# Optimization experiments

Measured on AMD Instinct MI355X. Metric: run time of the kernel, lower is better.

## Reference

```python
import jax, jax.numpy as jnp
import numpy as np

MODEL_DIM = 768
NUM_HEADS = 12
HEAD_DIM = MODEL_DIM // NUM_HEADS
TEMPERATURE = 1.0


def setup_inputs() -> dict:
    key = jax.random.key(0)
    ks = jax.random.split(key, 14)
    B, S, M, D = 4, 2048, 512, MODEL_DIM
    scale = 0.02
    return {
        "query_hidden_states": jax.random.normal(ks[0], (B, S, D), jnp.float32),
        "memory_embeddings": jax.random.normal(ks[1], (B, M, D), jnp.float32),
        "memory_scores": jax.random.normal(ks[2], (B, M), jnp.float32),
        "Wq": jax.random.normal(ks[3], (D, D), jnp.float32) * scale,
        "bq": jnp.zeros((D,), jnp.float32),
        "Wk": jax.random.normal(ks[4], (D, D), jnp.float32) * scale,
        "bk": jnp.zeros((D,), jnp.float32),
        "Wv": jax.random.normal(ks[5], (D, D), jnp.float32) * scale,
        "bv": jnp.zeros((D,), jnp.float32),
        "Wo": jax.random.normal(ks[6], (D, D), jnp.float32) * scale,
        "bo": jnp.zeros((D,), jnp.float32),
        "Wg": jax.random.normal(ks[7], (2 * D, D), jnp.float32) * scale,
        "bg": jnp.zeros((D,), jnp.float32),
    }


def reference(query_hidden_states, memory_embeddings, memory_scores,
              Wq, bq, Wk, bk, Wv, bv, Wo, bo, Wg, bg):
    B, S, D = query_hidden_states.shape
    M = memory_embeddings.shape[1]
    H, Hd = NUM_HEADS, HEAD_DIM

    q = query_hidden_states @ Wq + bq            # [B,S,D]
    k = memory_embeddings @ Wk + bk              # [B,M,D]
    v = memory_embeddings @ Wv + bv              # [B,M,D]

    q = q.reshape(B, S, H, Hd).transpose(0, 2, 1, 3) / jnp.sqrt(jnp.float32(Hd))
    k = k.reshape(B, M, H, Hd).transpose(0, 2, 1, 3)
    v = v.reshape(B, M, H, Hd).transpose(0, 2, 1, 3)

    scores = jnp.einsum('bhsd,bhmd->bhsm', q, k) / TEMPERATURE
    # additive memory-score bias broadcast over heads and query positions
    scores = scores + memory_scores[:, None, None, :]
    attn = jax.nn.softmax(scores, axis=-1)       # [B,H,S,M]

    out = jnp.einsum('bhsm,bhmd->bhsd', attn, v)
    out = out.transpose(0, 2, 1, 3).reshape(B, S, D)
    out = out @ Wo + bo                          # [B,S,D]

    concat = jnp.concatenate([query_hidden_states, out], axis=-1)  # [B,S,2D]
    gate = jax.nn.sigmoid(concat @ Wg + bg)
    return gate * out + (1.0 - gate) * query_hidden_states
```

## Files before the change

### kernel.cpp

```cpp
#include <hip/hip_runtime.h>
#include <hip/hip_bf16.h>

#define DEV static __device__ __forceinline__

typedef __attribute__((ext_vector_type(4))) float f32x4;
typedef __attribute__((ext_vector_type(8))) short bf16x8;

DEV unsigned short f2bf(float f) {
  union { float f; unsigned u; } v; v.f = f;
  unsigned r = (v.u + 0x7fffu + ((v.u >> 16) & 1u)) >> 16;
  return (unsigned short)r;
}
DEV float bf2f(unsigned short u) {
  union { unsigned u; float f; } v; v.u = ((unsigned)u) << 16;
  return v.f;
}
DEV void gl_lds16(const unsigned short* g, unsigned short* l) {
  __builtin_amdgcn_global_load_lds(
      (const __attribute__((address_space(1))) void*)g,
      (__attribute__((address_space(3))) void*)l, 16, 0, 0);
}

__global__ void k_cast2(const float* __restrict__ q, unsigned short* __restrict__ concat,
                        const float* __restrict__ mem, unsigned short* __restrict__ mem_bf) {
  int i = blockIdx.x * 256 + threadIdx.x;
  union { unsigned short u[4]; uint2 p; } o;
  if (i < 6144 * 256) {
    const int idx = i * 4;
    const int r = idx / 768, c = idx - r * 768;
    const float4 v = *(const float4*)(q + idx);
    o.u[0] = f2bf(v.x); o.u[1] = f2bf(v.y); o.u[2] = f2bf(v.z); o.u[3] = f2bf(v.w);
    *(uint2*)(concat + (size_t)r * 1536 + c) = o.p;
  } else {
    const int idx = (i - 6144 * 256) * 4;
    const float4 v = *(const float4*)(mem + idx);
    o.u[0] = f2bf(v.x); o.u[1] = f2bf(v.y); o.u[2] = f2bf(v.z); o.u[3] = f2bf(v.w);
    *(uint2*)(mem_bf + idx) = o.p;
  }
}

struct T6 {
  const float* src[6];
  unsigned short* dst[6];
  int ldd[6];
};
__global__ void k_transpose6(T6 d) {
  __shared__ float tile[32][33];
  const int z = blockIdx.z;
  const float* src = d.src[z];
  unsigned short* dst = d.dst[z];
  const int ldd = d.ldd[z];
  const int n0 = blockIdx.x * 32, k0 = blockIdx.y * 32;
  const int tx = threadIdx.x & 31, ty = threadIdx.x >> 5;
#pragma unroll
  for (int i = 0; i < 4; i++)
    tile[ty + i * 8][tx] = src[(size_t)(k0 + ty + i * 8) * 768 + n0 + tx];
  __syncthreads();
#pragma unroll
  for (int i = 0; i < 4; i++)
    dst[(size_t)(n0 + ty + i * 8) * ldd + k0 + tx] = f2bf(tile[tx][ty + i * 8]);
}

template <int EPI>
__global__ __launch_bounds__(256) void k_gemm(
    const unsigned short* __restrict__ A, int lda,
    const unsigned short* __restrict__ Bt, int ldb,
    const float* __restrict__ bias, const float* __restrict__ bias2,
    int K, float scale,
    unsigned short* __restrict__ out0, unsigned short* __restrict__ out1,
    const unsigned short* __restrict__ concat_in,
    const float* __restrict__ qy, float* __restrict__ dout, int gx) {
  __shared__ alignas(16) unsigned short Al[2][128 * 32];
  __shared__ alignas(16) unsigned short Bl[2][64 * 32];
  const int t = threadIdx.x;
  const int cpx = gridDim.x >> 3;
  const int swz = (blockIdx.x & 7) * cpx + (blockIdx.x >> 3);
  const int r0 = (swz / gx) * 128, c0 = (swz % gx) * 64;
  const int lane = t & 63, l15 = lane & 15, l4 = lane >> 4;
  const int wid = t >> 6, wr = wid >> 1, wc = wid & 1;

#define STAGE(buf, k0)                                                       \
  {                                                                          \
    _Pragma("unroll") for (int p = 0; p < 2; p++) {                          \
      const int flat = (p * 256 + t) * 8;                                    \
      gl_lds16(A + (size_t)(r0 + (flat >> 5)) * lda + (k0) + (flat & 31),    \
               &Al[buf][flat]);                                              \
    }                                                                        \
    const int fb = t * 8;                                                    \
    gl_lds16(Bt + (size_t)(c0 + (fb >> 5)) * ldb + (k0) + (fb & 31),         \
             &Bl[buf][fb]);                                                  \
  }

  f32x4 acc[4][2];
#pragma unroll
  for (int mi = 0; mi < 4; mi++)
#pragma unroll
    for (int ni = 0; ni < 2; ni++) acc[mi][ni] = (f32x4){0.f, 0.f, 0.f, 0.f};

  STAGE(0, 0);
  const int nt = K >> 5;
  for (int tk = 0; tk < nt; ++tk) {
    const int cur = tk & 1;
    __syncthreads();
    if (tk + 1 < nt) STAGE(cur ^ 1, (tk + 1) * 32);
    bf16x8 af[4], bfr[2];
#pragma unroll
    for (int mi = 0; mi < 4; mi++)
      af[mi] = *(const bf16x8*)&Al[cur][(wr * 64 + mi * 16 + l15) * 32 + l4 * 8];
#pragma unroll
    for (int ni = 0; ni < 2; ni++)
      bfr[ni] = *(const bf16x8*)&Bl[cur][(wc * 32 + ni * 16 + l15) * 32 + l4 * 8];
#pragma unroll
    for (int mi = 0; mi < 4; mi++)
#pragma unroll
      for (int ni = 0; ni < 2; ni++)
        acc[mi][ni] = __builtin_amdgcn_mfma_f32_16x16x32_bf16(af[mi], bfr[ni], acc[mi][ni], 0, 0, 0);
  }
#undef STAGE

#pragma unroll
  for (int ni = 0; ni < 2; ni++) {
    const int c = c0 + wc * 32 + ni * 16 + l15;
    const float bv = (EPI == 4 && c >= 768) ? bias2[c - 768] : bias[c];
#pragma unroll
    for (int mi = 0; mi < 4; mi++) {
      const int rbase = r0 + wr * 64 + mi * 16 + l4 * 4;
#pragma unroll
      for (int i = 0; i < 4; i++) {
        const int r = rbase + i;
        const float val = (acc[mi][ni][i] + bv) * scale;
        if (EPI == 0) {
          out0[(size_t)r * 768 + c] = f2bf(val);
        } else if (EPI == 2) {
          out0[(size_t)r * 1536 + 768 + c] = f2bf(val);
        } else if (EPI == 3) {
          const float g = 1.f / (1.f + __expf(-val));
          const float o = bf2f(concat_in[(size_t)r * 1536 + 768 + c]);
          const float q = qy[(size_t)r * 768 + c];
          dout[(size_t)r * 768 + c] = g * o + (1.f - g) * q;
        } else {
          if (c < 768) {
            out0[(size_t)r * 768 + c] = f2bf(val);
          } else {
            const int cc = c - 768;
            const int b = r >> 9, m = r & 511;
            const int h = cc >> 6, dd = cc & 63;
            out1[(((size_t)(b * 12 + h)) * 64 + dd) * 512 + m] = f2bf(val);
          }
        }
      }
    }
  }
}

__global__ __launch_bounds__(256, 3) void k_attn(
    const unsigned short* __restrict__ qbf,
    const unsigned short* __restrict__ kbf,
    const unsigned short* __restrict__ vT,
    const float* __restrict__ mscore,
    unsigned short* __restrict__ aout) {
  const int st = blockIdx.x, h = blockIdx.y, b = blockIdx.z;
  __shared__ float bias_s[512];
  __shared__ alignas(16) unsigned short Kl[128 * 64];
  __shared__ alignas(16) unsigned short Vl[64 * 128];
  __shared__ alignas(16) unsigned short P[4][16][136];
  const int t = threadIdx.x;
  const int wid = t >> 6, lane = t & 63, l15 = lane & 15, l4 = lane >> 4;
  for (int i = t; i < 512; i += 256) bias_s[i] = mscore[b * 512 + i];

  const int srow = st * 64 + wid * 16;
  const unsigned short* qrow = qbf + ((size_t)(b * 2048 + srow + l15)) * 768 + h * 64;
  bf16x8 qa[2];
  qa[0] = *(const bf16x8*)(qrow + l4 * 8);
  qa[1] = *(const bf16x8*)(qrow + 32 + l4 * 8);

  const unsigned short* kbase = kbf + (size_t)(b * 512) * 768 + h * 64;
  const unsigned short* vbase = vT + ((size_t)(b * 12 + h)) * 64 * 512;

  f32x4 O[4];
#pragma unroll
  for (int dt = 0; dt < 4; dt++) O[dt] = (f32x4){0.f, 0.f, 0.f, 0.f};
  float ml[4] = {-1e30f, -1e30f, -1e30f, -1e30f};
  float ll[4] = {0.f, 0.f, 0.f, 0.f};

  for (int ch = 0; ch < 4; ++ch) {
    const int m0 = ch * 128;
    __syncthreads();
#pragma unroll
    for (int j = 0; j < 4; ++j) {
      const int c = (j * 4 + wid) * 64 + lane;
      const int r = c >> 3, cc = c & 7;
      gl_lds16(kbase + (size_t)(m0 + r) * 768 + ((cc ^ (r & 7)) * 8), &Kl[c * 8]);
    }
#pragma unroll
    for (int j = 0; j < 4; ++j) {
      const int c = (j * 4 + wid) * 64 + lane;
      const int r = c >> 4, cc = c & 15;
      gl_lds16(vbase + (size_t)r * 512 + m0 + ((cc ^ (r & 7)) * 8), &Vl[c * 8]);
    }
    __syncthreads();

    f32x4 s8[8];
#pragma unroll
    for (int tt = 0; tt < 8; tt++) s8[tt] = (f32x4){0.f, 0.f, 0.f, 0.f};
#pragma unroll
    for (int kb = 0; kb < 2; kb++)
#pragma unroll
      for (int tt = 0; tt < 8; tt++) {
        const int r = tt * 16 + l15;
        const bf16x8 bb = *(const bf16x8*)&Kl[r * 64 + (((kb * 4 + l4) ^ (r & 7)) * 8)];
        s8[tt] = __builtin_amdgcn_mfma_f32_16x16x32_bf16(qa[kb], bb, s8[tt], 0, 0, 0);
      }

    float cm[4] = {-3e38f, -3e38f, -3e38f, -3e38f};
#pragma unroll
    for (int tt = 0; tt < 8; tt++) {
      const float bs = bias_s[m0 + tt * 16 + l15];
#pragma unroll
      for (int i = 0; i < 4; i++) {
        s8[tt][i] += bs;
        cm[i] = fmaxf(cm[i], s8[tt][i]);
      }
    }
#pragma unroll
    for (int d = 1; d < 16; d <<= 1)
#pragma unroll
      for (int i = 0; i < 4; i++) cm[i] = fmaxf(cm[i], __shfl_xor(cm[i], d));
    float mn[4], sc[4];
#pragma unroll
    for (int i = 0; i < 4; i++) {
      mn[i] = fmaxf(ml[i], cm[i]);
      sc[i] = __expf(ml[i] - mn[i]);
      ml[i] = mn[i];
      ll[i] *= sc[i];
    }
#pragma unroll
    for (int dt = 0; dt < 4; dt++)
#pragma unroll
      for (int i = 0; i < 4; i++) O[dt][i] *= sc[i];
    float rsum[4] = {0.f, 0.f, 0.f, 0.f};
#pragma unroll
    for (int tt = 0; tt < 8; tt++)
#pragma unroll
      for (int i = 0; i < 4; i++) {
        const float p = __expf(s8[tt][i] - mn[i]);
        rsum[i] += p;
        P[wid][l4 * 4 + i][tt * 16 + l15] = f2bf(p);
      }
#pragma unroll
    for (int d = 1; d < 16; d <<= 1)
#pragma unroll
      for (int i = 0; i < 4; i++) rsum[i] += __shfl_xor(rsum[i], d);
#pragma unroll
    for (int i = 0; i < 4; i++) ll[i] += rsum[i];

#pragma unroll
    for (int mk = 0; mk < 4; mk++) {
      const bf16x8 pa = *(const bf16x8*)&P[wid][l15][mk * 32 + l4 * 8];
#pragma unroll
      for (int dt = 0; dt < 4; dt++) {
        const int r = dt * 16 + l15;
        const bf16x8 vb = *(const bf16x8*)&Vl[r * 128 + (((mk * 4 + l4) ^ (r & 7)) * 8)];
        O[dt] = __builtin_amdgcn_mfma_f32_16x16x32_bf16(pa, vb, O[dt], 0, 0, 0);
      }
    }
  }

  float rinv[4];
#pragma unroll
  for (int i = 0; i < 4; i++) rinv[i] = 1.f / ll[i];
  const size_t rbase = (size_t)(b * 2048 + srow + l4 * 4);
#pragma unroll
  for (int dt = 0; dt < 4; dt++)
#pragma unroll
    for (int i = 0; i < 4; i++)
      aout[(rbase + i) * 768 + h * 64 + dt * 16 + l15] = f2bf(O[dt][i] * rinv[i]);
}

extern "C" void kernel_launch(void* const* d_in, const int* in_sizes, int n_in,
                              void* d_out, int out_size, void* d_ws, size_t ws_size,
                              hipStream_t stream) {
  const float* query  = (const float*)d_in[0];
  const float* memory = (const float*)d_in[1];
  const float* mscore = (const float*)d_in[2];
  const float* Wq = (const float*)d_in[3];
  const float* bq = (const float*)d_in[4];
  const float* Wk = (const float*)d_in[5];
  const float* bk = (const float*)d_in[6];
  const float* Wv = (const float*)d_in[7];
  const float* bv = (const float*)d_in[8];
  const float* Wo = (const float*)d_in[9];
  const float* bo = (const float*)d_in[10];
  const float* Wg = (const float*)d_in[11];
  const float* bg = (const float*)d_in[12];
  float* dout = (float*)d_out;

  char* ws = (char*)d_ws;
  unsigned short* concat = (unsigned short*)ws; ws += (size_t)8192 * 1536 * 2;
  unsigned short* mem_bf = (unsigned short*)ws; ws += (size_t)2048 * 768 * 2;
  unsigned short* Wqt = (unsigned short*)ws;    ws += (size_t)768 * 768 * 2;
  unsigned short* Wkvt = (unsigned short*)ws;   ws += (size_t)1536 * 768 * 2;
  unsigned short* Wot = (unsigned short*)ws;    ws += (size_t)768 * 768 * 2;
  unsigned short* Wgt = (unsigned short*)ws;    ws += (size_t)768 * 1536 * 2;
  unsigned short* q_bf = (unsigned short*)ws;   ws += (size_t)8192 * 768 * 2;
  unsigned short* k_bf = (unsigned short*)ws;   ws += (size_t)2048 * 768 * 2;
  unsigned short* vT = (unsigned short*)ws;     ws += (size_t)4 * 12 * 64 * 512 * 2;
  unsigned short* attn_bf = (unsigned short*)ws;

  k_cast2<<<7680, 256, 0, stream>>>(query, concat, memory, mem_bf);
  T6 td;
  td.src[0] = Wq;  td.dst[0] = Wqt;              td.ldd[0] = 768;
  td.src[1] = Wk;  td.dst[1] = Wkvt;             td.ldd[1] = 768;
  td.src[2] = Wv;  td.dst[2] = Wkvt + 768 * 768; td.ldd[2] = 768;
  td.src[3] = Wo;  td.dst[3] = Wot;              td.ldd[3] = 768;
  td.src[4] = Wg;  td.dst[4] = Wgt;              td.ldd[4] = 1536;
  td.src[5] = Wg + 768 * 768; td.dst[5] = Wgt + 768; td.ldd[5] = 1536;
  k_transpose6<<<dim3(24, 24, 6), 256, 0, stream>>>(td);

  k_gemm<0><<<64 * 12, 256, 0, stream>>>(concat, 1536, Wqt, 768, bq, nullptr, 768, 0.125f,
                                         q_bf, nullptr, nullptr, nullptr, nullptr, 12);
  k_gemm<4><<<16 * 24, 256, 0, stream>>>(mem_bf, 768, Wkvt, 768, bk, bv, 768, 1.f,
                                         k_bf, vT, nullptr, nullptr, nullptr, 24);
  k_attn<<<dim3(32, 12, 4), 256, 0, stream>>>(q_bf, k_bf, vT, mscore, attn_bf);
  k_gemm<2><<<64 * 12, 256, 0, stream>>>(attn_bf, 768, Wot, 768, bo, nullptr, 768, 1.f,
                                         concat, nullptr, nullptr, nullptr, nullptr, 12);
  k_gemm<3><<<64 * 12, 256, 0, stream>>>(concat, 1536, Wgt, 1536, bg, nullptr, 1536, 1.f,
                                         nullptr, nullptr, concat, query, dout, 12);
}
```

Before: 158.1 us.

## Deepen GEMM K-tile to 64 and XOR-swizzle LDS layout

Doubles the K-step of the bf16 MFMA GEMM from 32 to 64, halving the number of barrier-separated iterations, and adds an XOR swizzle of 16-byte chunks in LDS. The swizzle is applied on the global-address side because global_load_lds writes contiguously, and it is undone on the fragment reads. The aim is to remove LDS bank conflicts on the wider rows and amortize synchronization. LDS use doubles to about 48 KB per block, which may reduce occupancy, and K must now be a multiple of 64.

New measurement: 134.4 us. -15.0%, faster.

```diff
diff --git a/kernel.cpp b/kernel.cpp
--- a/kernel.cpp
+++ b/kernel.cpp
@@ -70,8 +70,8 @@
     unsigned short* __restrict__ out0, unsigned short* __restrict__ out1,
     const unsigned short* __restrict__ concat_in,
     const float* __restrict__ qy, float* __restrict__ dout, int gx) {
-  __shared__ alignas(16) unsigned short Al[2][128 * 32];
-  __shared__ alignas(16) unsigned short Bl[2][64 * 32];
+  __shared__ alignas(16) unsigned short Al[2][128 * 64];
+  __shared__ alignas(16) unsigned short Bl[2][64 * 64];
   const int t = threadIdx.x;
   const int cpx = gridDim.x >> 3;
   const int swz = (blockIdx.x & 7) * cpx + (blockIdx.x >> 3);
@@ -81,14 +81,18 @@
 
 #define STAGE(buf, k0)                                                       \
   {                                                                          \
+    _Pragma("unroll") for (int p = 0; p < 4; p++) {                          \
+      const int ch = p * 256 + t;                                            \
+      const int row = ch >> 3, s = ch & 7;                                   \
+      gl_lds16(A + (size_t)(r0 + row) * lda + (k0) + ((s ^ (row & 7)) * 8),  \
+               &Al[buf][ch * 8]);                                            \
+    }                                                                        \
     _Pragma("unroll") for (int p = 0; p < 2; p++) {                          \
-      const int flat = (p * 256 + t) * 8;                                    \
-      gl_lds16(A + (size_t)(r0 + (flat >> 5)) * lda + (k0) + (flat & 31),    \
-               &Al[buf][flat]);                                              \
+      const int ch = p * 256 + t;                                            \
+      const int row = ch >> 3, s = ch & 7;                                   \
+      gl_lds16(Bt + (size_t)(c0 + row) * ldb + (k0) + ((s ^ (row & 7)) * 8), \
+               &Bl[buf][ch * 8]);                                            \
     }                                                                        \
-    const int fb = t * 8;                                                    \
-    gl_lds16(Bt + (size_t)(c0 + (fb >> 5)) * ldb + (k0) + (fb & 31),         \
-             &Bl[buf][fb]);                                                  \
   }
 
   f32x4 acc[4][2];
@@ -98,23 +102,32 @@
     for (int ni = 0; ni < 2; ni++) acc[mi][ni] = (f32x4){0.f, 0.f, 0.f, 0.f};
 
   STAGE(0, 0);
-  const int nt = K >> 5;
+  const int nt = K >> 6;
   for (int tk = 0; tk < nt; ++tk) {
     const int cur = tk & 1;
     __syncthreads();
-    if (tk + 1 < nt) STAGE(cur ^ 1, (tk + 1) * 32);
-    bf16x8 af[4], bfr[2];
-#pragma unroll
-    for (int mi = 0; mi < 4; mi++)
-      af[mi] = *(const bf16x8*)&Al[cur][(wr * 64 + mi * 16 + l15) * 32 + l4 * 8];
-#pragma unroll
-    for (int ni = 0; ni < 2; ni++)
-      bfr[ni] = *(const bf16x8*)&Bl[cur][(wc * 32 + ni * 16 + l15) * 32 + l4 * 8];
-#pragma unroll
-    for (int mi = 0; mi < 4; mi++)
-#pragma unroll
-      for (int ni = 0; ni < 2; ni++)
-        acc[mi][ni] = __builtin_amdgcn_mfma_f32_16x16x32_bf16(af[mi], bfr[ni], acc[mi][ni], 0, 0, 0);
+    if (tk + 1 < nt) STAGE(cur ^ 1, (tk + 1) * 64);
+#pragma unroll
+    for (int kb = 0; kb < 2; kb++) {
+      bf16x8 af[4], bfr[2];
+#pragma unroll
+      for (int mi = 0; mi < 4; mi++) {
+        const int r = wr * 64 + mi * 16 + l15;
+        const int s = (kb * 4 + l4) ^ (r & 7);
+        af[mi] = *(const bf16x8*)&Al[cur][r * 64 + s * 8];
+      }
+#pragma unroll
+      for (int ni = 0; ni < 2; ni++) {
+        const int r = wc * 32 + ni * 16 + l15;
+        const int s = (kb * 4 + l4) ^ (r & 7);
+        bfr[ni] = *(const bf16x8*)&Bl[cur][r * 64 + s * 8];
+      }
+#pragma unroll
+      for (int mi = 0; mi < 4; mi++)
+#pragma unroll
+        for (int ni = 0; ni < 2; ni++)
+          acc[mi][ni] = __builtin_amdgcn_mfma_f32_16x16x32_bf16(af[mi], bfr[ni], acc[mi][ni], 0, 0, 0);
+    }
   }
 #undef STAGE
 
```
